# Kernel optimization log

Measured on AMD Instinct MI355X. Metric: run time of the kernel, lower is better.

## Reference

```python
import jax, jax.numpy as jnp
import numpy as np

# Dimensions: batch B, window W (time features), nodes M, hidden HID, hops NLAYERS
B, W, M, HID, NLAYERS = 32, 168, 2048, 128, 6


def setup_inputs() -> dict:
    key = jax.random.key(0)
    ks = jax.random.split(key, 6)
    x = jax.random.normal(ks[0], (B, W, M), dtype=jnp.float32)
    # scale L so matrix powers L^k stay bounded (spectral radius < 1)
    L = jax.random.normal(ks[1], (M, M), dtype=jnp.float32) / (2.0 * np.float32(np.sqrt(M)))
    # stacked per-hop MLP params: linears[i]: W->HID, linears2[i]: HID->1
    W1 = jax.random.normal(ks[2], (NLAYERS + 1, HID, W), dtype=jnp.float32) / np.float32(np.sqrt(W))
    b1 = jax.random.normal(ks[3], (NLAYERS + 1, HID), dtype=jnp.float32) * 0.01
    W2 = jax.random.normal(ks[4], (NLAYERS + 1, HID), dtype=jnp.float32) / np.float32(np.sqrt(HID))
    b2 = jax.random.normal(ks[5], (NLAYERS + 1,), dtype=jnp.float32) * 0.01
    return {"x": x, "L": L, "W1": W1, "b1": b1, "W2": W2, "b2": b2}


def _hop_mlp(t, w1, bb1, w2, bb2):
    # t: [B, M, W] -> scalar score per node: Linear(W->HID), ReLU, Linear(HID->1)
    h = jax.nn.relu(jnp.einsum('bmw,hw->bmh', t, w1) + bb1)
    return jnp.einsum('bmh,h->bm', h, w2) + bb2


def reference(x, L, W1, b1, W2, b2):
    xt = jnp.swapaxes(x, 1, 2)  # [B, M, W] (x.transpose(2,1))
    s = _hop_mlp(xt, W1[0], b1[0], W2[0], b2[0])  # [B, M]
    P = L
    for i in range(1, NLAYERS + 1):
        # PP.expand + bmm == broadcasted matmul; never materialize [B,M,M]
        t = jnp.einsum('ij,bjw->biw', P, xt)  # [B, M, W]
        s = s + _hop_mlp(t, W1[i], b1[i], W2[i], b2[i])
        P = jnp.matmul(L, P)  # next graph power
    return s  # [B, M]; output_fun is None so no final nonlinearity
```

## Files before the change

kernel.cpp:

```cpp
#include <hip/hip_runtime.h>
#include <cstdint>
#include <cstddef>

typedef __bf16 bf16_t;
typedef __attribute__((ext_vector_type(8))) __bf16 bf16x8;
typedef __attribute__((ext_vector_type(4))) __bf16 bf16x4;
typedef __attribute__((ext_vector_type(4))) float floatx4;

#define NB 32
#define NW 168
#define NM 2048
#define NHID 128
#define NBW (NB * NW)
#define GEMM_BLOCKS 672

#define GLOAD_LDS16(g, l)                                          \
  __builtin_amdgcn_global_load_lds(                                \
      (const __attribute__((address_space(1))) void*)(g),          \
      (__attribute__((address_space(3))) void*)(l), 16, 0, 0)

__global__ void prep_all(const float* __restrict__ x, bf16_t* __restrict__ Xb,
                         bf16_t* __restrict__ XT, const float* __restrict__ L,
                         bf16_t* __restrict__ Lb, const float* __restrict__ W1,
                         bf16_t* __restrict__ W1p) {
  __shared__ float tile[64][65];
  int bid = blockIdx.x;
  int t = threadIdx.x;
  if (bid < 2688) {
    const int C = NM;
    int r0 = (bid >> 5) * 64, c0 = (bid & 31) * 64;
    int tr = t >> 4, tc4 = (t & 15) * 4;
#pragma unroll
    for (int p = 0; p < 4; ++p) {
      int row = p * 16 + tr;
      float4 v = *(const float4*)(x + (size_t)(r0 + row) * C + c0 + tc4);
      tile[row][tc4 + 0] = v.x;
      tile[row][tc4 + 1] = v.y;
      tile[row][tc4 + 2] = v.z;
      tile[row][tc4 + 3] = v.w;
      bf16x4 o = {(bf16_t)v.x, (bf16_t)v.y, (bf16_t)v.z, (bf16_t)v.w};
      *(bf16x4*)(Xb + (size_t)(r0 + row) * C + c0 + tc4) = o;
    }
    __syncthreads();
#pragma unroll
    for (int p = 0; p < 4; ++p) {
      int c = p * 16 + tr;
      bf16x4 o = {(bf16_t)tile[tc4 + 0][c], (bf16_t)tile[tc4 + 1][c],
                  (bf16_t)tile[tc4 + 2][c], (bf16_t)tile[tc4 + 3][c]};
      *(bf16x4*)(XT + (size_t)(c0 + c) * NBW + r0 + tc4) = o;
    }
  } else if (bid < 3200) {
    int i = (bid - 2688) * 256 + t;
    const int n4 = NM * NM / 4;
    const int stride = 512 * 256;
    for (; i < n4; i += stride) {
      float4 v = ((const float4*)L)[i];
      bf16x4 o = {(bf16_t)v.x, (bf16_t)v.y, (bf16_t)v.z, (bf16_t)v.w};
      ((bf16x4*)Lb)[i] = o;
    }
  } else {
    int hop = bid - 3200;
    const float* src = W1 + (size_t)hop * NHID * NW;
    bf16_t* dst = W1p + (size_t)hop * NHID * 192;
    for (int c = t; c < 3072; c += 256) {
      int h = c / 24, kc = c % 24;
      bf16x8 o;
      if (kc < 21) {
        const float* s = src + (size_t)h * NW + kc * 8;
#pragma unroll
        for (int j = 0; j < 8; ++j) o[j] = (bf16_t)s[j];
      } else {
#pragma unroll
        for (int j = 0; j < 8; ++j) o[j] = (bf16_t)0.0f;
      }
      *(bf16x8*)(dst + (size_t)h * 192 + kc * 8) = o;
    }
  }
}

__global__ void fused_hop(const bf16_t* __restrict__ A, const bf16_t* __restrict__ Lb,
                          bf16_t* __restrict__ Tt, bf16_t* __restrict__ XTout,
                          const bf16_t* __restrict__ XTin, const bf16_t* __restrict__ W1p,
                          const float* __restrict__ b1, const float* __restrict__ W2,
                          const float* __restrict__ b2, float* __restrict__ out,
                          int hop, int accumulate, int gemm_blocks, int write_c) {
  __shared__ bf16_t As[128 * 32];
  __shared__ bf16_t Bs[128 * 32];
  __shared__ float sred[4][64];
  int tid = threadIdx.x;
  int lane = tid & 63, wv = tid >> 6;
  int wm = wv >> 1, wn = wv & 1;
  int quad = lane >> 4, l15 = lane & 15;
  floatx4 zero4 = {0.f, 0.f, 0.f, 0.f};
  floatx4 acc[4][4];
#pragma unroll
  for (int mi = 0; mi < 4; ++mi)
#pragma unroll
    for (int ni = 0; ni < 4; ++ni) acc[mi][ni] = zero4;

  if ((int)blockIdx.x < gemm_blocks) {
    int bid = blockIdx.x;
    int m0 = (bid >> 4) * 128, n0 = (bid & 15) * 128;
    int p0 = wv * 128 + lane;
    int p1 = p0 + 64;
    int row0 = p0 >> 2, kc0 = (p0 & 3) ^ ((p0 >> 3) & 3);
    int row1 = p1 >> 2, kc1 = (p1 & 3) ^ ((p1 >> 3) & 3);
    const bf16_t* a0p = A + (size_t)(m0 + row0) * NM + kc0 * 8;
    const bf16_t* a1p = A + (size_t)(m0 + row1) * NM + kc1 * 8;
    const bf16_t* b0p = Lb + (size_t)(n0 + row0) * NM + kc0 * 8;
    const bf16_t* b1p = Lb + (size_t)(n0 + row1) * NM + kc1 * 8;
    bf16_t* As_d0 = As + (size_t)(wv * 128) * 8;
    bf16_t* As_d1 = As + (size_t)(wv * 128 + 64) * 8;
    bf16_t* Bs_d0 = Bs + (size_t)(wv * 128) * 8;
    bf16_t* Bs_d1 = Bs + (size_t)(wv * 128 + 64) * 8;
    int swz = (l15 >> 1) & 3;
    int kpos = (quad ^ swz) * 8;

    for (int kb = 0; kb < 2048; kb += 32) {
      GLOAD_LDS16(a0p + kb, As_d0);
      GLOAD_LDS16(a1p + kb, As_d1);
      GLOAD_LDS16(b0p + kb, Bs_d0);
      GLOAD_LDS16(b1p + kb, Bs_d1);
      __syncthreads();
      bf16x8 af[4], bf[4];
#pragma unroll
      for (int mi = 0; mi < 4; ++mi)
        af[mi] = *(const bf16x8*)(As + (wm * 64 + mi * 16 + l15) * 32 + kpos);
#pragma unroll
      for (int ni = 0; ni < 4; ++ni)
        bf[ni] = *(const bf16x8*)(Bs + (wn * 64 + ni * 16 + l15) * 32 + kpos);
#pragma unroll
      for (int mi = 0; mi < 4; ++mi)
#pragma unroll
        for (int ni = 0; ni < 4; ++ni)
          acc[mi][ni] =
              __builtin_amdgcn_mfma_f32_16x16x32_bf16(af[mi], bf[ni], acc[mi][ni], 0, 0, 0);
      __syncthreads();
    }
#pragma unroll
    for (int mi = 0; mi < 4; ++mi) {
#pragma unroll
      for (int ni = 0; ni < 4; ++ni) {
        int col = n0 + wn * 64 + ni * 16 + l15;
        int rowb = m0 + wm * 64 + mi * 16 + quad * 4;
        bf16x4 tv;
#pragma unroll
        for (int r = 0; r < 4; ++r) tv[r] = (bf16_t)acc[mi][ni][r];
        *(bf16x4*)(XTout + (size_t)col * NBW + rowb) = tv;
        if (write_c) {
#pragma unroll
          for (int r = 0; r < 4; ++r) Tt[(size_t)(rowb + r) * NM + col] = tv[r];
        }
      }
    }
  } else {
    int bid2 = blockIdx.x - gemm_blocks;
    int r0 = bid2 * 128;
    const bf16_t* Wh = W1p + (size_t)hop * NHID * 192;
    const float* b1h = b1 + hop * NHID;
    const float* w2h = W2 + hop * NHID;
    const bf16_t* arow[4];
#pragma unroll
    for (int mi = 0; mi < 4; ++mi) {
      int R = r0 + wm * 64 + mi * 16 + l15;
      arow[mi] = XTin + (size_t)(R >> 5) * NBW + (size_t)(R & 31) * NW + quad * 8;
    }
#pragma unroll
    for (int kb = 0; kb < 192; kb += 32) {
      int kc = (kb >> 3) + quad;
      bf16x8 af[4], bf[4];
#pragma unroll
      for (int mi = 0; mi < 4; ++mi)
        af[mi] = *(const bf16x8*)(arow[mi] + kb);
#pragma unroll
      for (int ni = 0; ni < 4; ++ni) {
        int h = wn * 64 + ni * 16 + l15;
        bf[ni] = *(const bf16x8*)(Wh + (size_t)h * 192 + kc * 8);
      }
#pragma unroll
      for (int mi = 0; mi < 4; ++mi)
#pragma unroll
        for (int ni = 0; ni < 4; ++ni)
          acc[mi][ni] =
              __builtin_amdgcn_mfma_f32_16x16x32_bf16(af[mi], bf[ni], acc[mi][ni], 0, 0, 0);
    }
    float part[4][4];
#pragma unroll
    for (int mi = 0; mi < 4; ++mi)
#pragma unroll
      for (int r = 0; r < 4; ++r) part[mi][r] = 0.f;
#pragma unroll
    for (int ni = 0; ni < 4; ++ni) {
      int col = wn * 64 + ni * 16 + l15;
      float b1v = b1h[col];
      float w2v = w2h[col];
#pragma unroll
      for (int mi = 0; mi < 4; ++mi)
#pragma unroll
        for (int r = 0; r < 4; ++r) {
          float h = acc[mi][ni][r] + b1v;
          h = h > 0.f ? h : 0.f;
          part[mi][r] += h * w2v;
        }
    }
#pragma unroll
    for (int off = 1; off < 16; off <<= 1)
#pragma unroll
      for (int mi = 0; mi < 4; ++mi)
#pragma unroll
        for (int r = 0; r < 4; ++r) part[mi][r] += __shfl_xor(part[mi][r], off);
    if (l15 == 0) {
#pragma unroll
      for (int mi = 0; mi < 4; ++mi)
#pragma unroll
        for (int r = 0; r < 4; ++r) sred[wv][mi * 16 + quad * 4 + r] = part[mi][r];
    }
    __syncthreads();
    if (tid < 128) {
      int half = tid >> 6;
      int lr = tid & 63;
      float v = sred[half * 2][lr] + sred[half * 2 + 1][lr] + b2[hop];
      int R = r0 + half * 64 + lr;
      int idx = (R & 31) * NM + (R >> 5);
      if (accumulate)
        out[idx] += v;
      else
        out[idx] = v;
    }
  }
}

extern "C" void kernel_launch(void* const* d_in, const int* in_sizes, int n_in,
                              void* d_out, int out_size, void* d_ws, size_t ws_size,
                              hipStream_t stream) {
  const float* x = (const float*)d_in[0];
  const float* L = (const float*)d_in[1];
  const float* W1 = (const float*)d_in[2];
  const float* b1 = (const float*)d_in[3];
  const float* W2 = (const float*)d_in[4];
  const float* b2 = (const float*)d_in[5];
  float* out = (float*)d_out;

  char* ws = (char*)d_ws;
  size_t off = 0;
  auto walloc = [&](size_t bytes) -> void* {
    off = (off + 255) & ~(size_t)255;
    void* p = ws + off;
    off += bytes;
    return p;
  };
  const size_t SZ_T = (size_t)NBW * NM * 2;
  bf16_t* W1p = (bf16_t*)walloc((size_t)7 * NHID * 192 * 2);
  bf16_t* Lb = (bf16_t*)walloc((size_t)NM * NM * 2);
  bf16_t* Xb = (bf16_t*)walloc(SZ_T);
  bf16_t* Tta = (bf16_t*)walloc(SZ_T);
  bf16_t* Ttb = (bf16_t*)walloc(SZ_T);
  bf16_t* XTa = (bf16_t*)walloc(SZ_T);
  bf16_t* XTb = (bf16_t*)walloc(SZ_T);
  walloc(4096);
  (void)ws_size; (void)in_sizes; (void)n_in; (void)out_size;

  prep_all<<<dim3(3207), dim3(256), 0, stream>>>(x, Xb, XTa, L, Lb, W1, W1p);

  fused_hop<<<dim3(GEMM_BLOCKS + 512), dim3(256), 0, stream>>>(
      Xb, Lb, Tta, XTb, XTa, W1p, b1, W2, b2, out, 0, 0, GEMM_BLOCKS, 1);
  fused_hop<<<dim3(GEMM_BLOCKS + 512), dim3(256), 0, stream>>>(
      Tta, Lb, Ttb, XTa, XTb, W1p, b1, W2, b2, out, 1, 1, GEMM_BLOCKS, 1);
  fused_hop<<<dim3(GEMM_BLOCKS + 512), dim3(256), 0, stream>>>(
      Ttb, Lb, Tta, XTb, XTa, W1p, b1, W2, b2, out, 2, 1, GEMM_BLOCKS, 1);
  fused_hop<<<dim3(GEMM_BLOCKS + 512), dim3(256), 0, stream>>>(
      Tta, Lb, Ttb, XTa, XTb, W1p, b1, W2, b2, out, 3, 1, GEMM_BLOCKS, 1);
  fused_hop<<<dim3(GEMM_BLOCKS + 512), dim3(256), 0, stream>>>(
      Ttb, Lb, Tta, XTb, XTa, W1p, b1, W2, b2, out, 4, 1, GEMM_BLOCKS, 1);
  fused_hop<<<dim3(GEMM_BLOCKS + 512), dim3(256), 0, stream>>>(
      Tta, Lb, Ttb, XTa, XTb, W1p, b1, W2, b2, out, 5, 1, GEMM_BLOCKS, 0);
  fused_hop<<<dim3(512), dim3(256), 0, stream>>>(
      Ttb, Lb, Tta, XTb, XTa, W1p, b1, W2, b2, out, 6, 1, 0, 0);
}
```

Before: 563.2 us.

## Unfuse hop kernels, deepen GEMM K-tile, reassociate last hop through W1 projection

Splits the fused propagation/MLP kernel into separate GEMM and MLP kernels. The propagation GEMM now uses a 64-wide K tile, which halves the number of barrier iterations, and the MLP kernel stages W1 in LDS with a swizzle. For the final hop it projects x5 through W1 first (Zt = W1·x5 per batch), then multiplies L by Zt and fuses the bias, ReLU and W2 epilogue. This reassociation shrinks the inner dimension of the last propagation from 168 to 128 columns per batch. The split adds more kernel launches and gives up the previous overlap of GEMM and MLP work inside one launch.

```diff
diff --git a/kernel.cpp b/kernel.cpp
--- a/kernel.cpp
+++ b/kernel.cpp
@@ -11,8 +11,7 @@
 #define NW 168
 #define NM 2048
 #define NHID 128
-#define NBW (NB * NW)
-#define GEMM_BLOCKS 672
+#define NBW 5376
 
 #define GLOAD_LDS16(g, l)                                          \
   __builtin_amdgcn_global_load_lds(                                \
@@ -78,19 +77,97 @@
   }
 }
 
-__global__ void fused_hop(const bf16_t* __restrict__ A, const bf16_t* __restrict__ Lb,
-                          bf16_t* __restrict__ Tt, bf16_t* __restrict__ XTout,
-                          const bf16_t* __restrict__ XTin, const bf16_t* __restrict__ W1p,
-                          const float* __restrict__ b1, const float* __restrict__ W2,
-                          const float* __restrict__ b2, float* __restrict__ out,
-                          int hop, int accumulate, int gemm_blocks, int write_c) {
-  __shared__ bf16_t As[128 * 32];
-  __shared__ bf16_t Bs[128 * 32];
-  __shared__ float sred[4][64];
+__global__ void gemm_bk64(const bf16_t* __restrict__ A, const bf16_t* __restrict__ Lb,
+                          bf16_t* __restrict__ Tt, bf16_t* __restrict__ XTout, int write_c) {
+  __shared__ bf16_t As[128 * 64];
+  __shared__ bf16_t Bs[128 * 64];
+  int tid = threadIdx.x, bid = blockIdx.x;
+  int m0 = (bid >> 4) * 128, n0 = (bid & 15) * 128;
+  int lane = tid & 63, wv = tid >> 6;
+  int wm = wv >> 1, wn = wv & 1;
+  int quad = lane >> 4, l15 = lane & 15;
+
+  const bf16_t* apj[4];
+  const bf16_t* bpj[4];
+  bf16_t* adj[4];
+  bf16_t* bdj[4];
+#pragma unroll
+  for (int j = 0; j < 4; ++j) {
+    int p = wv * 256 + j * 64 + lane;
+    int r = p >> 3, c = (p & 7) ^ (r & 7);
+    apj[j] = A + (size_t)(m0 + r) * NM + c * 8;
+    bpj[j] = Lb + (size_t)(n0 + r) * NM + c * 8;
+    adj[j] = As + (size_t)(wv * 256 + j * 64) * 8;
+    bdj[j] = Bs + (size_t)(wv * 256 + j * 64) * 8;
+  }
+  int swz = l15 & 7;
+
+  floatx4 zero4 = {0.f, 0.f, 0.f, 0.f};
+  floatx4 acc[4][4];
+#pragma unroll
+  for (int mi = 0; mi < 4; ++mi)
+#pragma unroll
+    for (int ni = 0; ni < 4; ++ni) acc[mi][ni] = zero4;
+
+  for (int kb = 0; kb < 2048; kb += 64) {
+#pragma unroll
+    for (int j = 0; j < 4; ++j) GLOAD_LDS16(apj[j] + kb, adj[j]);
+#pragma unroll
+    for (int j = 0; j < 4; ++j) GLOAD_LDS16(bpj[j] + kb, bdj[j]);
+    __syncthreads();
+#pragma unroll
+    for (int h = 0; h < 2; ++h) {
+      bf16x8 af[4], bf[4];
+#pragma unroll
+      for (int mi = 0; mi < 4; ++mi)
+        af[mi] = *(const bf16x8*)(As + (wm * 64 + mi * 16 + l15) * 64 + (((h * 4 + quad) ^ swz) & 7) * 8);
+#pragma unroll
+      for (int ni = 0; ni < 4; ++ni)
+        bf[ni] = *(const bf16x8*)(Bs + (wn * 64 + ni * 16 + l15) * 64 + (((h * 4 + quad) ^ swz) & 7) * 8);
+#pragma unroll
+      for (int mi = 0; mi < 4; ++mi)
+#pragma unroll
+        for (int ni = 0; ni < 4; ++ni)
+          acc[mi][ni] = __builtin_amdgcn_mfma_f32_16x16x32_bf16(af[mi], bf[ni], acc[mi][ni], 0, 0, 0);
+    }
+    __syncthreads();
+  }
+#pragma unroll
+  for (int mi = 0; mi < 4; ++mi) {
+#pragma unroll
+    for (int ni = 0; ni < 4; ++ni) {
+      int col = n0 + wn * 64 + ni * 16 + l15;
+      int rowb = m0 + wm * 64 + mi * 16 + quad * 4;
+      bf16x4 tv;
+#pragma unroll
+      for (int r = 0; r < 4; ++r) tv[r] = (bf16_t)acc[mi][ni][r];
+      *(bf16x4*)(XTout + (size_t)col * NBW + rowb) = tv;
+      if (write_c) {
+#pragma unroll
+        for (int r = 0; r < 4; ++r) Tt[(size_t)(rowb + r) * NM + col] = tv[r];
+      }
+    }
+  }
+}
+
+__global__ void zproj(const bf16_t* __restrict__ XT5, const bf16_t* __restrict__ W1p,
+                      bf16_t* __restrict__ Zt) {
+  int bid = blockIdx.x;
+  int b = bid >> 4, n0 = (bid & 15) * 128;
+  const bf16_t* W6 = W1p + (size_t)6 * NHID * 192;
   int tid = threadIdx.x;
   int lane = tid & 63, wv = tid >> 6;
   int wm = wv >> 1, wn = wv & 1;
   int quad = lane >> 4, l15 = lane & 15;
+  const bf16_t* arow[4];
+  const bf16_t* brow[4];
+#pragma unroll
+  for (int mi = 0; mi < 4; ++mi)
+    arow[mi] = W6 + (size_t)(wm * 64 + mi * 16 + l15) * 192 + quad * 8;
+#pragma unroll
+  for (int ni = 0; ni < 4; ++ni)
+    brow[ni] = XT5 + (size_t)(n0 + wn * 64 + ni * 16 + l15) * NBW + b * NW + quad * 8;
+
   floatx4 zero4 = {0.f, 0.f, 0.f, 0.f};
   floatx4 acc[4][4];
 #pragma unroll
@@ -98,135 +175,233 @@
 #pragma unroll
     for (int ni = 0; ni < 4; ++ni) acc[mi][ni] = zero4;
 
-  if ((int)blockIdx.x < gemm_blocks) {
-    int bid = blockIdx.x;
-    int m0 = (bid >> 4) * 128, n0 = (bid & 15) * 128;
-    int p0 = wv * 128 + lane;
-    int p1 = p0 + 64;
-    int row0 = p0 >> 2, kc0 = (p0 & 3) ^ ((p0 >> 3) & 3);
-    int row1 = p1 >> 2, kc1 = (p1 & 3) ^ ((p1 >> 3) & 3);
-    const bf16_t* a0p = A + (size_t)(m0 + row0) * NM + kc0 * 8;
-    const bf16_t* a1p = A + (size_t)(m0 + row1) * NM + kc1 * 8;
-    const bf16_t* b0p = Lb + (size_t)(n0 + row0) * NM + kc0 * 8;
-    const bf16_t* b1p = Lb + (size_t)(n0 + row1) * NM + kc1 * 8;
-    bf16_t* As_d0 = As + (size_t)(wv * 128) * 8;
-    bf16_t* As_d1 = As + (size_t)(wv * 128 + 64) * 8;
-    bf16_t* Bs_d0 = Bs + (size_t)(wv * 128) * 8;
-    bf16_t* Bs_d1 = Bs + (size_t)(wv * 128 + 64) * 8;
-    int swz = (l15 >> 1) & 3;
-    int kpos = (quad ^ swz) * 8;
-
-    for (int kb = 0; kb < 2048; kb += 32) {
-      GLOAD_LDS16(a0p + kb, As_d0);
-      GLOAD_LDS16(a1p + kb, As_d1);
-      GLOAD_LDS16(b0p + kb, Bs_d0);
-      GLOAD_LDS16(b1p + kb, Bs_d1);
-      __syncthreads();
+#pragma unroll
+  for (int kb = 0; kb < 192; kb += 32) {
+    bf16x8 af[4], bf[4];
+#pragma unroll
+    for (int mi = 0; mi < 4; ++mi) af[mi] = *(const bf16x8*)(arow[mi] + kb);
+#pragma unroll
+    for (int ni = 0; ni < 4; ++ni) bf[ni] = *(const bf16x8*)(brow[ni] + kb);
+#pragma unroll
+    for (int mi = 0; mi < 4; ++mi)
+#pragma unroll
+      for (int ni = 0; ni < 4; ++ni)
+        acc[mi][ni] = __builtin_amdgcn_mfma_f32_16x16x32_bf16(af[mi], bf[ni], acc[mi][ni], 0, 0, 0);
+  }
+#pragma unroll
+  for (int mi = 0; mi < 4; ++mi) {
+#pragma unroll
+    for (int ni = 0; ni < 4; ++ni) {
+      int col = n0 + wn * 64 + ni * 16 + l15;
+      int rowb = b * 128 + wm * 64 + mi * 16 + quad * 4;
+#pragma unroll
+      for (int r = 0; r < 4; ++r)
+        Zt[(size_t)(rowb + r) * NM + col] = (bf16_t)acc[mi][ni][r];
+    }
+  }
+}
+
+__global__ void gemm_h6(const bf16_t* __restrict__ Lb, const bf16_t* __restrict__ Zt,
+                        const float* __restrict__ b1, const float* __restrict__ W2,
+                        const float* __restrict__ b2, float* __restrict__ out) {
+  __shared__ bf16_t As[128 * 64];
+  __shared__ bf16_t Bs[128 * 64];
+  __shared__ float sred[4][64];
+  int tid = threadIdx.x, bid = blockIdx.x;
+  int m0 = (bid >> 5) * 128, b = bid & 31;
+  int n0 = b * 128;
+  int lane = tid & 63, wv = tid >> 6;
+  int wm = wv >> 1, wn = wv & 1;
+  int quad = lane >> 4, l15 = lane & 15;
+
+  const bf16_t* apj[4];
+  const bf16_t* bpj[4];
+  bf16_t* adj[4];
+  bf16_t* bdj[4];
+#pragma unroll
+  for (int j = 0; j < 4; ++j) {
+    int p = wv * 256 + j * 64 + lane;
+    int r = p >> 3, c = (p & 7) ^ (r & 7);
+    apj[j] = Lb + (size_t)(m0 + r) * NM + c * 8;
+    bpj[j] = Zt + (size_t)(n0 + r) * NM + c * 8;
+    adj[j] = As + (size_t)(wv * 256 + j * 64) * 8;
+    bdj[j] = Bs + (size_t)(wv * 256 + j * 64) * 8;
+  }
+  int swz = l15 & 7;
+
+  floatx4 zero4 = {0.f, 0.f, 0.f, 0.f};
+  floatx4 acc[4][4];
+#pragma unroll
+  for (int mi = 0; mi < 4; ++mi)
+#pragma unroll
+    for (int ni = 0; ni < 4; ++ni) acc[mi][ni] = zero4;
+
+  for (int kb = 0; kb < 2048; kb += 64) {
+#pragma unroll
+    for (int j = 0; j < 4; ++j) GLOAD_LDS16(apj[j] + kb, adj[j]);
+#pragma unroll
+    for (int j = 0; j < 4; ++j) GLOAD_LDS16(bpj[j] + kb, bdj[j]);
+    __syncthreads();
+#pragma unroll
+    for (int h = 0; h < 2; ++h) {
       bf16x8 af[4], bf[4];
 #pragma unroll
       for (int mi = 0; mi < 4; ++mi)
-        af[mi] = *(const bf16x8*)(As + (wm * 64 + mi * 16 + l15) * 32 + kpos);
+        af[mi] = *(const bf16x8*)(As + (wm * 64 + mi * 16 + l15) * 64 + (((h * 4 + quad) ^ swz) & 7) * 8);
 #pragma unroll
       for (int ni = 0; ni < 4; ++ni)
-        bf[ni] = *(const bf16x8*)(Bs + (wn * 64 + ni * 16 + l15) * 32 + kpos);
+        bf[ni] = *(const bf16x8*)(Bs + (wn * 64 + ni * 16 + l15) * 64 + (((h * 4 + quad) ^ swz) & 7) * 8);
 #pragma unroll
       for (int mi = 0; mi < 4; ++mi)
 #pragma unroll
         for (int ni = 0; ni < 4; ++ni)
-          acc[mi][ni] =
-              __builtin_amdgcn_mfma_f32_16x16x32_bf16(af[mi], bf[ni], acc[mi][ni], 0, 0, 0);
-      __syncthreads();
-    }
-#pragma unroll
-    for (int mi = 0; mi < 4; ++mi) {
-#pragma unroll
-      for (int ni = 0; ni < 4; ++ni) {
-        int col = n0 + wn * 64 + ni * 16 + l15;
-        int rowb = m0 + wm * 64 + mi * 16 + quad * 4;
-        bf16x4 tv;
-#pragma unroll
-        for (int r = 0; r < 4; ++r) tv[r] = (bf16_t)acc[mi][ni][r];
-        *(bf16x4*)(XTout + (size_t)col * NBW + rowb) = tv;
-        if (write_c) {
-#pragma unroll
-          for (int r = 0; r < 4; ++r) Tt[(size_t)(rowb + r) * NM + col] = tv[r];
-        }
+          acc[mi][ni] = __builtin_amdgcn_mfma_f32_16x16x32_bf16(af[mi], bf[ni], acc[mi][ni], 0, 0, 0);
+    }
+    __syncthreads();
+  }
+
+  const float* b1h = b1 + 6 * NHID;
+  const float* w2h = W2 + 6 * NHID;
+  float part[4][4];
+#pragma unroll
+  for (int mi = 0; mi < 4; ++mi)
+#pragma unroll
+    for (int r = 0; r < 4; ++r) part[mi][r] = 0.f;
+#pragma unroll
+  for (int ni = 0; ni < 4; ++ni) {
+    int col = wn * 64 + ni * 16 + l15;
+    float b1v = b1h[col];
+    float w2v = w2h[col];
+#pragma unroll
+    for (int mi = 0; mi < 4; ++mi)
+#pragma unroll
+      for (int r = 0; r < 4; ++r) {
+        float hh = acc[mi][ni][r] + b1v;
+        hh = hh > 0.f ? hh : 0.f;
+        part[mi][r] += hh * w2v;
       }
-    }
-  } else {
-    int bid2 = blockIdx.x - gemm_blocks;
-    int r0 = bid2 * 128;
-    const bf16_t* Wh = W1p + (size_t)hop * NHID * 192;
-    const float* b1h = b1 + hop * NHID;
-    const float* w2h = W2 + hop * NHID;
-    const bf16_t* arow[4];
-#pragma unroll
-    for (int mi = 0; mi < 4; ++mi) {
-      int R = r0 + wm * 64 + mi * 16 + l15;
-      arow[mi] = XTin + (size_t)(R >> 5) * NBW + (size_t)(R & 31) * NW + quad * 8;
-    }
-#pragma unroll
-    for (int kb = 0; kb < 192; kb += 32) {
-      int kc = (kb >> 3) + quad;
-      bf16x8 af[4], bf[4];
-#pragma unroll
-      for (int mi = 0; mi < 4; ++mi)
-        af[mi] = *(const bf16x8*)(arow[mi] + kb);
-#pragma unroll
-      for (int ni = 0; ni < 4; ++ni) {
-        int h = wn * 64 + ni * 16 + l15;
-        bf[ni] = *(const bf16x8*)(Wh + (size_t)h * 192 + kc * 8);
+  }
+#pragma unroll
+  for (int off = 1; off < 16; off <<= 1)
+#pragma unroll
+    for (int mi = 0; mi < 4; ++mi)
+#pragma unroll
+      for (int r = 0; r < 4; ++r) part[mi][r] += __shfl_xor(part[mi][r], off);
+  if (l15 == 0) {
+#pragma unroll
+    for (int mi = 0; mi < 4; ++mi)
+#pragma unroll
+      for (int r = 0; r < 4; ++r) sred[wv][mi * 16 + quad * 4 + r] = part[mi][r];
+  }
+  __syncthreads();
+  if (tid < 128) {
+    int half = tid >> 6;
+    int lr = tid & 63;
+    float v = sred[half * 2][lr] + sred[half * 2 + 1][lr] + b2[6];
+    out[(size_t)b * NM + m0 + half * 64 + lr] += v;
+  }
+}
+
+__global__ void mlp_score(const bf16_t* __restrict__ XT, const bf16_t* __restrict__ W1p,
+                          const float* __restrict__ b1, const float* __restrict__ W2,
+                          const float* __restrict__ b2, float* __restrict__ out,
+                          int hop, int accumulate) {
+  __shared__ bf16_t Bs[24 * 128 * 8];
+  __shared__ float sred[4][64];
+  const bf16_t* Wh = W1p + (size_t)hop * NHID * 192;
+  const float* b1h = b1 + hop * NHID;
+  const float* w2h = W2 + hop * NHID;
+  int tid = threadIdx.x;
+  int r0 = blockIdx.x * 128;
+  int lane = tid & 63, wv = tid >> 6;
+  int wm = wv >> 1, wn = wv & 1;
+  int quad = lane >> 4, l15 = lane & 15;
+
+#pragma unroll
+  for (int i = 0; i < 12; ++i) {
+    int c = i * 256 + tid;
+    int kc = c >> 7;
+    int h = (c & 127) ^ ((kc & 3) << 2);
+    GLOAD_LDS16(Wh + (size_t)h * 192 + kc * 8, Bs + (size_t)(i * 256 + wv * 64) * 8);
+  }
+
+  const bf16_t* arow[4];
+#pragma unroll
+  for (int mi = 0; mi < 4; ++mi) {
+    int R = r0 + wm * 64 + mi * 16 + l15;
+    arow[mi] = XT + (size_t)(R >> 5) * NBW + (size_t)(R & 31) * NW + quad * 8;
+  }
+
+  floatx4 zero4 = {0.f, 0.f, 0.f, 0.f};
+  floatx4 acc[4][4];
+#pragma unroll
+  for (int mi = 0; mi < 4; ++mi)
+#pragma unroll
+    for (int ni = 0; ni < 4; ++ni) acc[mi][ni] = zero4;
+
+  __syncthreads();
+
+#pragma unroll
+  for (int kb = 0; kb < 192; kb += 32) {
+    int kc = (kb >> 3) + quad;
+    bf16x8 af[4], bf[4];
+#pragma unroll
+    for (int mi = 0; mi < 4; ++mi)
+      af[mi] = *(const bf16x8*)(arow[mi] + kb);
+#pragma unroll
+    for (int ni = 0; ni < 4; ++ni) {
+      int hpos = (wn * 64 + ni * 16 + l15) ^ ((kc & 3) << 2);
+      bf[ni] = *(const bf16x8*)(Bs + (size_t)(kc * 128 + hpos) * 8);
+    }
+#pragma unroll
+    for (int mi = 0; mi < 4; ++mi)
+#pragma unroll
+      for (int ni = 0; ni < 4; ++ni)
+        acc[mi][ni] = __builtin_amdgcn_mfma_f32_16x16x32_bf16(af[mi], bf[ni], acc[mi][ni], 0, 0, 0);
+  }
+
+  float part[4][4];
+#pragma unroll
+  for (int mi = 0; mi < 4; ++mi)
+#pragma unroll
+    for (int r = 0; r < 4; ++r) part[mi][r] = 0.f;
+#pragma unroll
+  for (int ni = 0; ni < 4; ++ni) {
+    int col = wn * 64 + ni * 16 + l15;
+    float b1v = b1h[col];
+    float w2v = w2h[col];
+#pragma unroll
+    for (int mi = 0; mi < 4; ++mi)
+#pragma unroll
+      for (int r = 0; r < 4; ++r) {
+        float h = acc[mi][ni][r] + b1v;
+        h = h > 0.f ? h : 0.f;
+        part[mi][r] += h * w2v;
       }
-#pragma unroll
-      for (int mi = 0; mi < 4; ++mi)
-#pragma unroll
-        for (int ni = 0; ni < 4; ++ni)
-          acc[mi][ni] =
-              __builtin_amdgcn_mfma_f32_16x16x32_bf16(af[mi], bf[ni], acc[mi][ni], 0, 0, 0);
-    }
-    float part[4][4];
-#pragma unroll
-    for (int mi = 0; mi < 4; ++mi)
-#pragma unroll
-      for (int r = 0; r < 4; ++r) part[mi][r] = 0.f;
-#pragma unroll
-    for (int ni = 0; ni < 4; ++ni) {
-      int col = wn * 64 + ni * 16 + l15;
-      float b1v = b1h[col];
-      float w2v = w2h[col];
-#pragma unroll
-      for (int mi = 0; mi < 4; ++mi)
-#pragma unroll
-        for (int r = 0; r < 4; ++r) {
-          float h = acc[mi][ni][r] + b1v;
-          h = h > 0.f ? h : 0.f;
-          part[mi][r] += h * w2v;
-        }
-    }
-#pragma unroll
-    for (int off = 1; off < 16; off <<= 1)
-#pragma unroll
-      for (int mi = 0; mi < 4; ++mi)
-#pragma unroll
-        for (int r = 0; r < 4; ++r) part[mi][r] += __shfl_xor(part[mi][r], off);
-    if (l15 == 0) {
-#pragma unroll
-      for (int mi = 0; mi < 4; ++mi)
-#pragma unroll
-        for (int r = 0; r < 4; ++r) sred[wv][mi * 16 + quad * 4 + r] = part[mi][r];
-    }
-    __syncthreads();
-    if (tid < 128) {
-      int half = tid >> 6;
-      int lr = tid & 63;
-      float v = sred[half * 2][lr] + sred[half * 2 + 1][lr] + b2[hop];
-      int R = r0 + half * 64 + lr;
-      int idx = (R & 31) * NM + (R >> 5);
-      if (accumulate)
-        out[idx] += v;
-      else
-        out[idx] = v;
-    }
+  }
+#pragma unroll
+  for (int off = 1; off < 16; off <<= 1)
+#pragma unroll
+    for (int mi = 0; mi < 4; ++mi)
+#pragma unroll
+      for (int r = 0; r < 4; ++r) part[mi][r] += __shfl_xor(part[mi][r], off);
+  if (l15 == 0) {
+#pragma unroll
+    for (int mi = 0; mi < 4; ++mi)
+#pragma unroll
+      for (int r = 0; r < 4; ++r) sred[wv][mi * 16 + quad * 4 + r] = part[mi][r];
+  }
+  __syncthreads();
+  if (tid < 128) {
+    int half = tid >> 6;
+    int lr = tid & 63;
+    float v = sred[half * 2][lr] + sred[half * 2 + 1][lr] + b2[hop];
+    int R = r0 + half * 64 + lr;
+    int idx = (R & 31) * NM + (R >> 5);
+    if (accumulate)
+      out[idx] += v;
+    else
+      out[idx] = v;
   }
 }
 
@@ -257,23 +432,25 @@
   bf16_t* Ttb = (bf16_t*)walloc(SZ_T);
   bf16_t* XTa = (bf16_t*)walloc(SZ_T);
   bf16_t* XTb = (bf16_t*)walloc(SZ_T);
+  bf16_t* Zt = (bf16_t*)walloc((size_t)4096 * NM * 2);
   walloc(4096);
   (void)ws_size; (void)in_sizes; (void)n_in; (void)out_size;
 
   prep_all<<<dim3(3207), dim3(256), 0, stream>>>(x, Xb, XTa, L, Lb, W1, W1p);
 
-  fused_hop<<<dim3(GEMM_BLOCKS + 512), dim3(256), 0, stream>>>(
-      Xb, Lb, Tta, XTb, XTa, W1p, b1, W2, b2, out, 0, 0, GEMM_BLOCKS, 1);
-  fused_hop<<<dim3(GEMM_BLOCKS + 512), dim3(256), 0, stream>>>(
-      Tta, Lb, Ttb, XTa, XTb, W1p, b1, W2, b2, out, 1, 1, GEMM_BLOCKS, 1);
-  fused_hop<<<dim3(GEMM_BLOCKS + 512), dim3(256), 0, stream>>>(
-      Ttb, Lb, Tta, XTb, XTa, W1p, b1, W2, b2, out, 2, 1, GEMM_BLOCKS, 1);
-  fused_hop<<<dim3(GEMM_BLOCKS + 512), dim3(256), 0, stream>>>(
-      Tta, Lb, Ttb, XTa, XTb, W1p, b1, W2, b2, out, 3, 1, GEMM_BLOCKS, 1);
-  fused_hop<<<dim3(GEMM_BLOCKS + 512), dim3(256), 0, stream>>>(
-      Ttb, Lb, Tta, XTb, XTa, W1p, b1, W2, b2, out, 4, 1, GEMM_BLOCKS, 1);
-  fused_hop<<<dim3(GEMM_BLOCKS + 512), dim3(256), 0, stream>>>(
-      Tta, Lb, Ttb, XTa, XTb, W1p, b1, W2, b2, out, 5, 1, GEMM_BLOCKS, 0);
-  fused_hop<<<dim3(512), dim3(256), 0, stream>>>(
-      Ttb, Lb, Tta, XTb, XTa, W1p, b1, W2, b2, out, 6, 1, 0, 0);
-}
+  mlp_score<<<dim3(512), dim3(256), 0, stream>>>(XTa, W1p, b1, W2, b2, out, 0, 0);
+
+  gemm_bk64<<<dim3(672), dim3(256), 0, stream>>>(Xb, Lb, Tta, XTb, 1);
+  mlp_score<<<dim3(512), dim3(256), 0, stream>>>(XTb, W1p, b1, W2, b2, out, 1, 1);
+  gemm_bk64<<<dim3(672), dim3(256), 0, stream>>>(Tta, Lb, Ttb, XTa, 1);
+  mlp_score<<<dim3(512), dim3(256), 0, stream>>>(XTa, W1p, b1, W2, b2, out, 2, 1);
+  gemm_bk64<<<dim3(672), dim3(256), 0, stream>>>(Ttb, Lb, Tta, XTb, 1);
+  mlp_score<<<dim3(512), dim3(256), 0, stream>>>(XTb, W1p, b1, W2, b2, out, 3, 1);
+  gemm_bk64<<<dim3(672), dim3(256), 0, stream>>>(Tta, Lb, Ttb, XTa, 1);
+  mlp_score<<<dim3(512), dim3(256), 0, stream>>>(XTa, W1p, b1, W2, b2, out, 4, 1);
+  gemm_bk64<<<dim3(672), dim3(256), 0, stream>>>(Ttb, Lb, nullptr, XTb, 0);
+  mlp_score<<<dim3(512), dim3(256), 0, stream>>>(XTb, W1p, b1, W2, b2, out, 5, 1);
+
+  zproj<<<dim3(512), dim3(256), 0, stream>>>(XTb, W1p, Zt);
+  gemm_h6<<<dim3(512), dim3(256), 0, stream>>>(Lb, Zt, b1, W2, b2, out);
+}
```

New measurement: 710.4 us. 26.1% more time.

## Reassociate hops: project X by W1 first, then multiply by precomputed powers of L

Applied to the files above, without the earlier changes.

Reorders the computation so each hop first projects X with W1 (Z = W1·X, dimension 128 instead of 168), then multiplies by L^k, whose powers are built with a squaring schedule (L2, L3, L4, L5, L6) spread across five dependency-staged kernels. GEMMs from different stages are packed into the same launches, and the scores are accumulated with atomics. This cuts the inner dimension of the large per-hop GEMMs and shortens the serial chain of launches. The cost is extra M×M power GEMMs, more workspace, atomic adds to the output, and additional bf16 rounding through the chain of L powers.

```diff
diff --git a/kernel.cpp b/kernel.cpp
--- a/kernel.cpp
+++ b/kernel.cpp
@@ -11,35 +11,54 @@
 #define NW 168
 #define NM 2048
 #define NHID 128
-#define NBW (NB * NW)
-#define GEMM_BLOCKS 672
+#define NBW 5376
 
 #define GLOAD_LDS16(g, l)                                          \
   __builtin_amdgcn_global_load_lds(                                \
       (const __attribute__((address_space(1))) void*)(g),          \
       (__attribute__((address_space(3))) void*)(l), 16, 0, 0)
 
-__global__ void prep_all(const float* __restrict__ x, bf16_t* __restrict__ Xb,
-                         bf16_t* __restrict__ XT, const float* __restrict__ L,
-                         bf16_t* __restrict__ Lb, const float* __restrict__ W1,
+__global__ void prep_all(const float* __restrict__ x, bf16_t* __restrict__ XT,
+                         const float* __restrict__ L, bf16_t* __restrict__ Lb,
+                         bf16_t* __restrict__ Ltb, const float* __restrict__ W1,
                          bf16_t* __restrict__ W1p) {
   __shared__ float tile[64][65];
   int bid = blockIdx.x;
   int t = threadIdx.x;
   if (bid < 2688) {
-    const int C = NM;
     int r0 = (bid >> 5) * 64, c0 = (bid & 31) * 64;
     int tr = t >> 4, tc4 = (t & 15) * 4;
 #pragma unroll
     for (int p = 0; p < 4; ++p) {
       int row = p * 16 + tr;
-      float4 v = *(const float4*)(x + (size_t)(r0 + row) * C + c0 + tc4);
+      float4 v = *(const float4*)(x + (size_t)(r0 + row) * NM + c0 + tc4);
+      tile[row][tc4 + 0] = v.x;
+      tile[row][tc4 + 1] = v.y;
+      tile[row][tc4 + 2] = v.z;
+      tile[row][tc4 + 3] = v.w;
+    }
+    __syncthreads();
+#pragma unroll
+    for (int p = 0; p < 4; ++p) {
+      int c = p * 16 + tr;
+      bf16x4 o = {(bf16_t)tile[tc4 + 0][c], (bf16_t)tile[tc4 + 1][c],
+                  (bf16_t)tile[tc4 + 2][c], (bf16_t)tile[tc4 + 3][c]};
+      *(bf16x4*)(XT + (size_t)(c0 + c) * NBW + r0 + tc4) = o;
+    }
+  } else if (bid < 3712) {
+    int l = bid - 2688;
+    int r0 = (l >> 5) * 64, c0 = (l & 31) * 64;
+    int tr = t >> 4, tc4 = (t & 15) * 4;
+#pragma unroll
+    for (int p = 0; p < 4; ++p) {
+      int row = p * 16 + tr;
+      float4 v = *(const float4*)(L + (size_t)(r0 + row) * NM + c0 + tc4);
       tile[row][tc4 + 0] = v.x;
       tile[row][tc4 + 1] = v.y;
       tile[row][tc4 + 2] = v.z;
       tile[row][tc4 + 3] = v.w;
       bf16x4 o = {(bf16_t)v.x, (bf16_t)v.y, (bf16_t)v.z, (bf16_t)v.w};
-      *(bf16x4*)(Xb + (size_t)(r0 + row) * C + c0 + tc4) = o;
+      *(bf16x4*)(Lb + (size_t)(r0 + row) * NM + c0 + tc4) = o;
     }
     __syncthreads();
 #pragma unroll
@@ -47,19 +66,10 @@
       int c = p * 16 + tr;
       bf16x4 o = {(bf16_t)tile[tc4 + 0][c], (bf16_t)tile[tc4 + 1][c],
                   (bf16_t)tile[tc4 + 2][c], (bf16_t)tile[tc4 + 3][c]};
-      *(bf16x4*)(XT + (size_t)(c0 + c) * NBW + r0 + tc4) = o;
-    }
-  } else if (bid < 3200) {
-    int i = (bid - 2688) * 256 + t;
-    const int n4 = NM * NM / 4;
-    const int stride = 512 * 256;
-    for (; i < n4; i += stride) {
-      float4 v = ((const float4*)L)[i];
-      bf16x4 o = {(bf16_t)v.x, (bf16_t)v.y, (bf16_t)v.z, (bf16_t)v.w};
-      ((bf16x4*)Lb)[i] = o;
+      *(bf16x4*)(Ltb + (size_t)(c0 + c) * NM + r0 + tc4) = o;
     }
   } else {
-    int hop = bid - 3200;
+    int hop = bid - 3712;
     const float* src = W1 + (size_t)hop * NHID * NW;
     bf16_t* dst = W1p + (size_t)hop * NHID * 192;
     for (int c = t; c < 3072; c += 256) {
@@ -78,129 +88,205 @@
   }
 }
 
-__global__ void fused_hop(const bf16_t* __restrict__ A, const bf16_t* __restrict__ Lb,
-                          bf16_t* __restrict__ Tt, bf16_t* __restrict__ XTout,
-                          const bf16_t* __restrict__ XTin, const bf16_t* __restrict__ W1p,
-                          const float* __restrict__ b1, const float* __restrict__ W2,
-                          const float* __restrict__ b2, float* __restrict__ out,
-                          int hop, int accumulate, int gemm_blocks, int write_c) {
+__global__ void score0(const bf16_t* __restrict__ Z0, const float* __restrict__ b1,
+                       const float* __restrict__ W2, const float* __restrict__ b2,
+                       float* __restrict__ out) {
+  __shared__ float sred[2][128];
+  int bid = blockIdx.x;
+  int b = bid >> 4, mt = bid & 15;
+  int t = threadIdx.x;
+  int c = t & 127, rh = t >> 7;
+  const bf16_t* base = Z0 + (size_t)b * 128 * 2048 + mt * 128 + c;
+  float acc = 0.f;
+  for (int h = rh; h < 128; h += 2) {
+    float z = (float)base[(size_t)h * 2048];
+    float v = z + b1[h];
+    v = v > 0.f ? v : 0.f;
+    acc += v * W2[h];
+  }
+  sred[rh][c] = acc;
+  __syncthreads();
+  if (t < 128) out[(size_t)b * NM + mt * 128 + c] = sred[0][c] + sred[1][c] + b2[0];
+}
+
+template <int D>
+__global__ void mega(const bf16_t* __restrict__ XT, const bf16_t* __restrict__ W1p,
+                     const bf16_t* __restrict__ Lb, const bf16_t* __restrict__ Ltb,
+                     bf16_t* __restrict__ L2t, bf16_t* __restrict__ L2,
+                     bf16_t* __restrict__ L3, bf16_t* __restrict__ L4,
+                     bf16_t* __restrict__ L5, bf16_t* __restrict__ L6,
+                     bf16_t* __restrict__ Z, const float* __restrict__ b1,
+                     const float* __restrict__ W2, const float* __restrict__ b2,
+                     float* __restrict__ out) {
   __shared__ bf16_t As[128 * 32];
   __shared__ bf16_t Bs[128 * 32];
   __shared__ float sred[4][64];
-  int tid = threadIdx.x;
+  const size_t ZS = (size_t)4096 * 2048;
+  int bid = blockIdx.x, tid = threadIdx.x;
   int lane = tid & 63, wv = tid >> 6;
   int wm = wv >> 1, wn = wv & 1;
   int quad = lane >> 4, l15 = lane & 15;
-  floatx4 zero4 = {0.f, 0.f, 0.f, 0.f};
-  floatx4 acc[4][4];
-#pragma unroll
-  for (int mi = 0; mi < 4; ++mi)
-#pragma unroll
-    for (int ni = 0; ni < 4; ++ni) acc[mi][ni] = zero4;
-
-  if ((int)blockIdx.x < gemm_blocks) {
-    int bid = blockIdx.x;
-    int m0 = (bid >> 4) * 128, n0 = (bid & 15) * 128;
-    int p0 = wv * 128 + lane;
-    int p1 = p0 + 64;
-    int row0 = p0 >> 2, kc0 = (p0 & 3) ^ ((p0 >> 3) & 3);
-    int row1 = p1 >> 2, kc1 = (p1 & 3) ^ ((p1 >> 3) & 3);
-    const bf16_t* a0p = A + (size_t)(m0 + row0) * NM + kc0 * 8;
-    const bf16_t* a1p = A + (size_t)(m0 + row1) * NM + kc1 * 8;
-    const bf16_t* b0p = Lb + (size_t)(n0 + row0) * NM + kc0 * 8;
-    const bf16_t* b1p = Lb + (size_t)(n0 + row1) * NM + kc1 * 8;
-    bf16_t* As_d0 = As + (size_t)(wv * 128) * 8;
-    bf16_t* As_d1 = As + (size_t)(wv * 128 + 64) * 8;
-    bf16_t* Bs_d0 = Bs + (size_t)(wv * 128) * 8;
-    bf16_t* Bs_d1 = Bs + (size_t)(wv * 128 + 64) * 8;
-    int swz = (l15 >> 1) & 3;
-    int kpos = (quad ^ swz) * 8;
-
-    for (int kb = 0; kb < 2048; kb += 32) {
-      GLOAD_LDS16(a0p + kb, As_d0);
-      GLOAD_LDS16(a1p + kb, As_d1);
-      GLOAD_LDS16(b0p + kb, Bs_d0);
-      GLOAD_LDS16(b1p + kb, Bs_d1);
-      __syncthreads();
+
+  int jt, hop = 0, lb = 0;
+  const bf16_t* A = nullptr;
+  const bf16_t* Bt = nullptr;
+  bf16_t* C = nullptr;
+  bf16_t* Ct = nullptr;
+  if constexpr (D == 1) {
+    if (bid < 256)       { jt = 0; lb = bid;        A = Lb; Bt = Ltb; C = L2; Ct = L2t; }
+    else                 { jt = 2; int z = bid - 256;  hop = z >> 9;       lb = z & 511; }
+  } else if constexpr (D == 2) {
+    if (bid < 256)       { jt = 0; lb = bid;        A = L2; Bt = Ltb; C = L3; }
+    else if (bid < 512)  { jt = 0; lb = bid - 256;  A = L2; Bt = L2t; C = L4; }
+    else if (bid < 1024) { jt = 1; lb = bid - 512;  A = Lb; Bt = Z + 1 * ZS; hop = 1; }
+    else                 { jt = 2; int z = bid - 1024; hop = 2 + (z >> 9); lb = z & 511; }
+  } else if constexpr (D == 3) {
+    if (bid < 256)       { jt = 0; lb = bid;        A = L3; Bt = L2t; C = L5; }
+    else if (bid < 512)  { jt = 0; lb = bid - 256;  A = L4; Bt = L2t; C = L6; }
+    else if (bid < 1024) { jt = 1; lb = bid - 512;  A = L2; Bt = Z + 2 * ZS; hop = 2; }
+    else if (bid < 1536) { jt = 1; lb = bid - 1024; A = L3; Bt = Z + 3 * ZS; hop = 3; }
+    else                 { jt = 2; int z = bid - 1536; hop = 4 + (z >> 9); lb = z & 511; }
+  } else if constexpr (D == 4) {
+    if (bid < 512)       { jt = 1; lb = bid;        A = L4; Bt = Z + 0 * ZS; hop = 4; }
+    else if (bid < 1024) { jt = 1; lb = bid - 512;  A = L5; Bt = Z + 1 * ZS; hop = 5; }
+    else                 { jt = 2; int z = bid - 1024; hop = 6;            lb = z; }
+  } else {
+    jt = 1; lb = bid; A = L6; Bt = Z + 2 * ZS; hop = 6;
+  }
+
+  if (jt == 2) {
+    int b = lb >> 4, n0 = (lb & 15) * 128;
+    const bf16_t* Wh = W1p + (size_t)hop * (NHID * 192);
+    bf16_t* Zc = Z + (size_t)(hop & 3) * ZS;
+    const bf16_t* arow[4];
+    const bf16_t* brow[4];
+#pragma unroll
+    for (int mi = 0; mi < 4; ++mi)
+      arow[mi] = Wh + (size_t)(wm * 64 + mi * 16 + l15) * 192 + quad * 8;
+#pragma unroll
+    for (int ni = 0; ni < 4; ++ni)
+      brow[ni] = XT + (size_t)(n0 + wn * 64 + ni * 16 + l15) * NBW + b * NW + quad * 8;
+    floatx4 zero4 = {0.f, 0.f, 0.f, 0.f};
+    floatx4 acc[4][4];
+#pragma unroll
+    for (int mi = 0; mi < 4; ++mi)
+#pragma unroll
+      for (int ni = 0; ni < 4; ++ni) acc[mi][ni] = zero4;
+#pragma unroll
+    for (int kb = 0; kb < 192; kb += 32) {
       bf16x8 af[4], bf[4];
 #pragma unroll
-      for (int mi = 0; mi < 4; ++mi)
-        af[mi] = *(const bf16x8*)(As + (wm * 64 + mi * 16 + l15) * 32 + kpos);
-#pragma unroll
-      for (int ni = 0; ni < 4; ++ni)
-        bf[ni] = *(const bf16x8*)(Bs + (wn * 64 + ni * 16 + l15) * 32 + kpos);
+      for (int mi = 0; mi < 4; ++mi) af[mi] = *(const bf16x8*)(arow[mi] + kb);
+#pragma unroll
+      for (int ni = 0; ni < 4; ++ni) bf[ni] = *(const bf16x8*)(brow[ni] + kb);
 #pragma unroll
       for (int mi = 0; mi < 4; ++mi)
 #pragma unroll
         for (int ni = 0; ni < 4; ++ni)
           acc[mi][ni] =
               __builtin_amdgcn_mfma_f32_16x16x32_bf16(af[mi], bf[ni], acc[mi][ni], 0, 0, 0);
-      __syncthreads();
     }
 #pragma unroll
     for (int mi = 0; mi < 4; ++mi) {
 #pragma unroll
       for (int ni = 0; ni < 4; ++ni) {
         int col = n0 + wn * 64 + ni * 16 + l15;
+        int rowb = b * 128 + wm * 64 + mi * 16 + quad * 4;
+#pragma unroll
+        for (int r = 0; r < 4; ++r)
+          Zc[(size_t)(rowb + r) * 2048 + col] = (bf16_t)acc[mi][ni][r];
+      }
+    }
+    return;
+  }
+
+  int m0, nrow0, b = 0;
+  if (jt == 0) {
+    m0 = (lb >> 4) * 128;
+    nrow0 = (lb & 15) * 128;
+  } else {
+    m0 = (lb >> 5) * 128;
+    b = lb & 31;
+    nrow0 = b * 128;
+  }
+  int p0 = wv * 128 + lane;
+  int p1 = p0 + 64;
+  int row0 = p0 >> 2, kc0 = (p0 & 3) ^ ((p0 >> 3) & 3);
+  int row1 = p1 >> 2, kc1 = (p1 & 3) ^ ((p1 >> 3) & 3);
+  const bf16_t* a0p = A + (size_t)(m0 + row0) * NM + kc0 * 8;
+  const bf16_t* a1p = A + (size_t)(m0 + row1) * NM + kc1 * 8;
+  const bf16_t* b0p = Bt + (size_t)(nrow0 + row0) * NM + kc0 * 8;
+  const bf16_t* b1p = Bt + (size_t)(nrow0 + row1) * NM + kc1 * 8;
+  bf16_t* As_d0 = As + (size_t)(wv * 128) * 8;
+  bf16_t* As_d1 = As + (size_t)(wv * 128 + 64) * 8;
+  bf16_t* Bs_d0 = Bs + (size_t)(wv * 128) * 8;
+  bf16_t* Bs_d1 = Bs + (size_t)(wv * 128 + 64) * 8;
+  int swz = (l15 >> 1) & 3;
+  int kpos = (quad ^ swz) * 8;
+
+  floatx4 zero4 = {0.f, 0.f, 0.f, 0.f};
+  floatx4 acc[4][4];
+#pragma unroll
+  for (int mi = 0; mi < 4; ++mi)
+#pragma unroll
+    for (int ni = 0; ni < 4; ++ni) acc[mi][ni] = zero4;
+
+  for (int kb = 0; kb < 2048; kb += 32) {
+    GLOAD_LDS16(a0p + kb, As_d0);
+    GLOAD_LDS16(a1p + kb, As_d1);
+    GLOAD_LDS16(b0p + kb, Bs_d0);
+    GLOAD_LDS16(b1p + kb, Bs_d1);
+    __syncthreads();
+    bf16x8 af[4], bf[4];
+#pragma unroll
+    for (int mi = 0; mi < 4; ++mi)
+      af[mi] = *(const bf16x8*)(As + (wm * 64 + mi * 16 + l15) * 32 + kpos);
+#pragma unroll
+    for (int ni = 0; ni < 4; ++ni)
+      bf[ni] = *(const bf16x8*)(Bs + (wn * 64 + ni * 16 + l15) * 32 + kpos);
+#pragma unroll
+    for (int mi = 0; mi < 4; ++mi)
+#pragma unroll
+      for (int ni = 0; ni < 4; ++ni)
+        acc[mi][ni] = __builtin_amdgcn_mfma_f32_16x16x32_bf16(af[mi], bf[ni], acc[mi][ni], 0, 0, 0);
+    __syncthreads();
+  }
+
+  if (jt == 0) {
+#pragma unroll
+    for (int mi = 0; mi < 4; ++mi) {
+#pragma unroll
+      for (int ni = 0; ni < 4; ++ni) {
+        int col = nrow0 + wn * 64 + ni * 16 + l15;
         int rowb = m0 + wm * 64 + mi * 16 + quad * 4;
         bf16x4 tv;
 #pragma unroll
         for (int r = 0; r < 4; ++r) tv[r] = (bf16_t)acc[mi][ni][r];
-        *(bf16x4*)(XTout + (size_t)col * NBW + rowb) = tv;
-        if (write_c) {
-#pragma unroll
-          for (int r = 0; r < 4; ++r) Tt[(size_t)(rowb + r) * NM + col] = tv[r];
-        }
+#pragma unroll
+        for (int r = 0; r < 4; ++r) C[(size_t)(rowb + r) * NM + col] = tv[r];
+        if (Ct) *(bf16x4*)(Ct + (size_t)col * NM + rowb) = tv;
       }
     }
   } else {
-    int bid2 = blockIdx.x - gemm_blocks;
-    int r0 = bid2 * 128;
-    const bf16_t* Wh = W1p + (size_t)hop * NHID * 192;
     const float* b1h = b1 + hop * NHID;
     const float* w2h = W2 + hop * NHID;
-    const bf16_t* arow[4];
-#pragma unroll
-    for (int mi = 0; mi < 4; ++mi) {
-      int R = r0 + wm * 64 + mi * 16 + l15;
-      arow[mi] = XTin + (size_t)(R >> 5) * NBW + (size_t)(R & 31) * NW + quad * 8;
-    }
-#pragma unroll
-    for (int kb = 0; kb < 192; kb += 32) {
-      int kc = (kb >> 3) + quad;
-      bf16x8 af[4], bf[4];
+    float part[4][4];
+#pragma unroll
+    for (int mi = 0; mi < 4; ++mi)
+#pragma unroll
+      for (int r = 0; r < 4; ++r) part[mi][r] = 0.f;
+#pragma unroll
+    for (int ni = 0; ni < 4; ++ni) {
+      int h = wn * 64 + ni * 16 + l15;
+      float b1v = b1h[h];
+      float w2v = w2h[h];
 #pragma unroll
       for (int mi = 0; mi < 4; ++mi)
-        af[mi] = *(const bf16x8*)(arow[mi] + kb);
-#pragma unroll
-      for (int ni = 0; ni < 4; ++ni) {
-        int h = wn * 64 + ni * 16 + l15;
-        bf[ni] = *(const bf16x8*)(Wh + (size_t)h * 192 + kc * 8);
-      }
-#pragma unroll
-      for (int mi = 0; mi < 4; ++mi)
-#pragma unroll
-        for (int ni = 0; ni < 4; ++ni)
-          acc[mi][ni] =
-              __builtin_amdgcn_mfma_f32_16x16x32_bf16(af[mi], bf[ni], acc[mi][ni], 0, 0, 0);
-    }
-    float part[4][4];
-#pragma unroll
-    for (int mi = 0; mi < 4; ++mi)
-#pragma unroll
-      for (int r = 0; r < 4; ++r) part[mi][r] = 0.f;
-#pragma unroll
-    for (int ni = 0; ni < 4; ++ni) {
-      int col = wn * 64 + ni * 16 + l15;
-      float b1v = b1h[col];
-      float w2v = w2h[col];
-#pragma unroll
-      for (int mi = 0; mi < 4; ++mi)
 #pragma unroll
         for (int r = 0; r < 4; ++r) {
-          float h = acc[mi][ni][r] + b1v;
-          h = h > 0.f ? h : 0.f;
-          part[mi][r] += h * w2v;
+          float hh = acc[mi][ni][r] + b1v;
+          hh = hh > 0.f ? hh : 0.f;
+          part[mi][r] += hh * w2v;
         }
     }
 #pragma unroll
@@ -220,12 +306,7 @@
       int half = tid >> 6;
       int lr = tid & 63;
       float v = sred[half * 2][lr] + sred[half * 2 + 1][lr] + b2[hop];
-      int R = r0 + half * 64 + lr;
-      int idx = (R & 31) * NM + (R >> 5);
-      if (accumulate)
-        out[idx] += v;
-      else
-        out[idx] = v;
+      atomicAdd(out + (size_t)b * NM + m0 + half * 64 + lr, v);
     }
   }
 }
@@ -249,31 +330,32 @@
     off += bytes;
     return p;
   };
-  const size_t SZ_T = (size_t)NBW * NM * 2;
+  const size_t SZ_L = (size_t)NM * NM * 2;
   bf16_t* W1p = (bf16_t*)walloc((size_t)7 * NHID * 192 * 2);
-  bf16_t* Lb = (bf16_t*)walloc((size_t)NM * NM * 2);
-  bf16_t* Xb = (bf16_t*)walloc(SZ_T);
-  bf16_t* Tta = (bf16_t*)walloc(SZ_T);
-  bf16_t* Ttb = (bf16_t*)walloc(SZ_T);
-  bf16_t* XTa = (bf16_t*)walloc(SZ_T);
-  bf16_t* XTb = (bf16_t*)walloc(SZ_T);
+  bf16_t* XT = (bf16_t*)walloc((size_t)NM * NBW * 2);
+  bf16_t* Lb = (bf16_t*)walloc(SZ_L);
+  bf16_t* Ltb = (bf16_t*)walloc(SZ_L);
+  bf16_t* L2t = (bf16_t*)walloc(SZ_L);
+  bf16_t* L2 = (bf16_t*)walloc(SZ_L);
+  bf16_t* L3 = (bf16_t*)walloc(SZ_L);
+  bf16_t* L4 = (bf16_t*)walloc(SZ_L);
+  bf16_t* L6 = (bf16_t*)walloc(SZ_L);
+  bf16_t* L5 = Ltb;
+  bf16_t* Z = (bf16_t*)walloc((size_t)4 * 4096 * 2048 * 2);
   walloc(4096);
   (void)ws_size; (void)in_sizes; (void)n_in; (void)out_size;
 
-  prep_all<<<dim3(3207), dim3(256), 0, stream>>>(x, Xb, XTa, L, Lb, W1, W1p);
-
-  fused_hop<<<dim3(GEMM_BLOCKS + 512), dim3(256), 0, stream>>>(
-      Xb, Lb, Tta, XTb, XTa, W1p, b1, W2, b2, out, 0, 0, GEMM_BLOCKS, 1);
-  fused_hop<<<dim3(GEMM_BLOCKS + 512), dim3(256), 0, stream>>>(
-      Tta, Lb, Ttb, XTa, XTb, W1p, b1, W2, b2, out, 1, 1, GEMM_BLOCKS, 1);
-  fused_hop<<<dim3(GEMM_BLOCKS + 512), dim3(256), 0, stream>>>(
-      Ttb, Lb, Tta, XTb, XTa, W1p, b1, W2, b2, out, 2, 1, GEMM_BLOCKS, 1);
-  fused_hop<<<dim3(GEMM_BLOCKS + 512), dim3(256), 0, stream>>>(
-      Tta, Lb, Ttb, XTa, XTb, W1p, b1, W2, b2, out, 3, 1, GEMM_BLOCKS, 1);
-  fused_hop<<<dim3(GEMM_BLOCKS + 512), dim3(256), 0, stream>>>(
-      Ttb, Lb, Tta, XTb, XTa, W1p, b1, W2, b2, out, 4, 1, GEMM_BLOCKS, 1);
-  fused_hop<<<dim3(GEMM_BLOCKS + 512), dim3(256), 0, stream>>>(
-      Tta, Lb, Ttb, XTa, XTb, W1p, b1, W2, b2, out, 5, 1, GEMM_BLOCKS, 0);
-  fused_hop<<<dim3(512), dim3(256), 0, stream>>>(
-      Ttb, Lb, Tta, XTb, XTa, W1p, b1, W2, b2, out, 6, 1, 0, 0);
+  prep_all<<<dim3(3719), dim3(256), 0, stream>>>(x, XT, L, Lb, Ltb, W1, W1p);
+
+  mega<1><<<dim3(1280), dim3(256), 0, stream>>>(XT, W1p, Lb, Ltb, L2t, L2, L3, L4, L5, L6, Z,
+                                                b1, W2, b2, out);
+  score0<<<dim3(512), dim3(256), 0, stream>>>(Z, b1, W2, b2, out);
+  mega<2><<<dim3(2048), dim3(256), 0, stream>>>(XT, W1p, Lb, Ltb, L2t, L2, L3, L4, L5, L6, Z,
+                                                b1, W2, b2, out);
+  mega<3><<<dim3(2560), dim3(256), 0, stream>>>(XT, W1p, Lb, Ltb, L2t, L2, L3, L4, L5, L6, Z,
+                                                b1, W2, b2, out);
+  mega<4><<<dim3(1536), dim3(256), 0, stream>>>(XT, W1p, Lb, Ltb, L2t, L2, L3, L4, L5, L6, Z,
+                                                b1, W2, b2, out);
+  mega<5><<<dim3(512), dim3(256), 0, stream>>>(XT, W1p, Lb, Ltb, L2t, L2, L3, L4, L5, L6, Z,
+                                               b1, W2, b2, out);
 }
```

Result: no change. 560.9 us (-0.4%).
